# Optimization experiments

Hardware: AMD Instinct MI355X
Metric: run time of the kernel (lower is better)

## Reference

```python
import jax, jax.numpy as jnp
import numpy as np

K = 3
K2 = K * K
PAD = (K - 1) // 2
DECAY_RATE = 4.0
REL_THRESHOLD = 0.3
EPS = 1e-8


def _deform_sample(depth, offset):
    """Deformable bilinear gather equivalent to the fixed-identity-weight
    ModulatedDeformConv2d (mask=1, bias=0). Returns [B, K2, H, W]."""
    B, _, H, W = depth.shape
    d = depth[:, 0]  # [B, H, W]
    dt = depth.dtype
    # mmcv offset layout: channel 2*i = dy, 2*i+1 = dx for kernel point i
    off = offset.reshape(B, K2, 2, H, W)
    off_y, off_x = off[:, :, 0], off[:, :, 1]          # [B, K2, H, W]
    ky = (jnp.arange(K2) // K - PAD).astype(dt)        # [K2]
    kx = (jnp.arange(K2) % K - PAD).astype(dt)
    ys = jnp.arange(H, dtype=dt)
    xs = jnp.arange(W, dtype=dt)
    # sampling locations: p = base_pixel + kernel_offset + learned_offset
    py = off_y + ys[None, None, :, None] + ky[None, :, None, None]  # [B,K2,H,W]
    px = off_x + xs[None, None, None, :] + kx[None, :, None, None]
    y0 = jnp.floor(py)
    x0 = jnp.floor(px)
    wy = py - y0  # bilinear weights
    wx = px - x0
    y0i = y0.astype(jnp.int32)
    x0i = x0.astype(jnp.int32)

    def gather(iy, ix):
        # zero-padded gather (matches mmcv out-of-bounds handling)
        valid = (iy >= 0) & (iy < H) & (ix >= 0) & (ix < W)
        iyc = jnp.clip(iy, 0, H - 1)
        ixc = jnp.clip(ix, 0, W - 1)
        vals = jax.vmap(lambda img, a, b: img[a, b])(d, iyc, ixc)  # [B,K2,H,W]
        return jnp.where(valid, vals, jnp.zeros((), dt))

    v00 = gather(y0i, x0i)
    v01 = gather(y0i, x0i + 1)
    v10 = gather(y0i + 1, x0i)
    v11 = gather(y0i + 1, x0i + 1)
    return (v00 * (1 - wy) * (1 - wx) + v01 * (1 - wy) * wx
            + v10 * wy * (1 - wx) + v11 * wy * wx)


def setup_inputs() -> dict:
    key = jax.random.key(0)
    k1, k2 = jax.random.split(key)
    B, H, W = 8, 480, 640
    depth = jax.random.uniform(k1, (B, 1, H, W), dtype=jnp.float32)
    offset = jax.random.normal(k2, (B, 2 * K2, H, W), dtype=jnp.float32)
    return {"depth": depth, "offset": offset}


def reference(depth, offset):
    sampled = _deform_sample(depth, offset)           # [B, K2, H, W]
    center = sampled[:, K2 // 2: K2 // 2 + 1]         # [B, 1, H, W]
    depth_diff = jnp.abs(sampled - center)
    # normalize_mode == 'threshold' (default path)
    relative_diff = depth_diff / (center + EPS)
    within = relative_diff <= REL_THRESHOLD
    affinity = jnp.exp(-DECAY_RATE * (depth_diff - center * REL_THRESHOLD))
    return jnp.where(within, jnp.ones_like(affinity), affinity)
```

## Files before the change

### kernel.cpp

```cpp
#include <hip/hip_runtime.h>

constexpr int KK = 3;
constexpr int K2 = 9;
constexpr int PADC = 1;
constexpr float DECAY = 4.0f;
constexpr float RELT = 0.3f;
constexpr float EPSV = 1e-8f;
constexpr int H = 480;
constexpr int W = 640;
constexpr int HW = H * W;

typedef float f32x4 __attribute__((ext_vector_type(4)));

constexpr int TH = 16;
constexpr int TW = 64;
constexpr int PADT = 8;
constexpr int LR = TH + 2 * PADT;
constexpr int LC = TW + 2 * PADT;
constexpr int LSTRIDE = LC + 1;
constexpr int NSTAGE = LR * LC;

__device__ __forceinline__ float dsample(const float* __restrict__ img, int iy, int ix) {
    bool valid = (iy >= 0) & (iy < H) & (ix >= 0) & (ix < W);
    int iyc = min(max(iy, 0), H - 1);
    int ixc = min(max(ix, 0), W - 1);
    float v = img[iyc * W + ixc];
    return valid ? v : 0.0f;
}

__device__ __forceinline__ void tap4(const float* __restrict__ tile,
                                     const float* __restrict__ dimg,
                                     int by0, int bx0, int r, int col,
                                     f32x4 oy, f32x4 ox, int ky, int kx,
                                     float* s4) {
    int y0[4], x0[4];
    float wy[4], wx[4];
    bool fast = true;
#pragma unroll
    for (int j = 0; j < 4; ++j) {
        float pyt = oy[j] + (float)(r + PADT + ky);
        float pxt = ox[j] + (float)(col + j + PADT + kx);
        float y0f = floorf(pyt);
        float x0f = floorf(pxt);
        wy[j] = pyt - y0f;
        wx[j] = pxt - x0f;
        y0[j] = (int)y0f;
        x0[j] = (int)x0f;
        fast &= ((unsigned)y0[j] < (unsigned)(LR - 1)) & ((unsigned)x0[j] < (unsigned)(LC - 1));
    }
    if (fast) {
#pragma unroll
        for (int j = 0; j < 4; ++j) {
            int a = y0[j] * LSTRIDE + x0[j];
            float v00 = tile[a];
            float v01 = tile[a + 1];
            float v10 = tile[a + LSTRIDE];
            float v11 = tile[a + LSTRIDE + 1];
            float wy1 = 1.0f - wy[j];
            float wx1 = 1.0f - wx[j];
            s4[j] = v00 * wy1 * wx1 + v01 * wy1 * wx[j] + v10 * wy[j] * wx1 + v11 * wy[j] * wx[j];
        }
    } else {
#pragma unroll
        for (int j = 0; j < 4; ++j) {
            int gy = y0[j] + by0 - PADT;
            int gx = x0[j] + bx0 - PADT;
            float v00 = dsample(dimg, gy, gx);
            float v01 = dsample(dimg, gy, gx + 1);
            float v10 = dsample(dimg, gy + 1, gx);
            float v11 = dsample(dimg, gy + 1, gx + 1);
            float wy1 = 1.0f - wy[j];
            float wx1 = 1.0f - wx[j];
            s4[j] = v00 * wy1 * wx1 + v01 * wy1 * wx[j] + v10 * wy[j] * wx1 + v11 * wy[j] * wx[j];
        }
    }
}

__global__ __launch_bounds__(256) void affinity_kernel(
    const float* __restrict__ depth,
    const float* __restrict__ offset,
    float* __restrict__ out)
{
    const int bx0 = blockIdx.x * TW;
    const int by0 = blockIdx.y * TH;
    const int b   = blockIdx.z;
    const int t   = threadIdx.x;

    __shared__ float tile[LR * LSTRIDE];

    const float* __restrict__ dimg = depth + (size_t)b * HW;

    const int col = (t & 15) * 4;
    const int r   = t >> 4;
    const int y   = by0 + r;
    const int x   = bx0 + col;

    const size_t obase = ((size_t)b * 2 * K2) * HW + (size_t)y * W + x;
    const float* __restrict__ offp = offset + obase;

    constexpr int ORD[K2] = {4, 0, 1, 2, 3, 5, 6, 7, 8};

    f32x4 oyc = *reinterpret_cast<const f32x4*>(offp + (size_t)(2 * ORD[0]) * HW);
    f32x4 oxc = *reinterpret_cast<const f32x4*>(offp + (size_t)(2 * ORD[0] + 1) * HW);

#pragma unroll
    for (int i = 0; i < NSTAGE / 256; ++i) {
        int idx = t + i * 256;
        int rr = idx / LC;
        int cc = idx - rr * LC;
        int yi = by0 - PADT + rr;
        int xi = bx0 - PADT + cc;
        float v = 0.0f;
        if ((unsigned)yi < (unsigned)H && (unsigned)xi < (unsigned)W)
            v = dimg[yi * W + xi];
        tile[rr * LSTRIDE + cc] = v;
    }
    __syncthreads();

    float* __restrict__ outp = out + ((size_t)b * K2) * HW + (size_t)y * W + x;

    float c4[4], thr[4], cr[4];

#pragma unroll
    for (int i = 0; i < K2; ++i) {
        const int k = ORD[i];
        f32x4 oyn, oxn;
        if (i + 1 < K2) {
            oyn = *reinterpret_cast<const f32x4*>(offp + (size_t)(2 * ORD[i + 1]) * HW);
            oxn = *reinterpret_cast<const f32x4*>(offp + (size_t)(2 * ORD[i + 1] + 1) * HW);
        }

        float s4[4];
        tap4(tile, dimg, by0, bx0, r, col, oyc, oxc, k / KK - PADC, k % KK - PADC, s4);

        if (i == 0) {
#pragma unroll
            for (int j = 0; j < 4; ++j) {
                c4[j]  = s4[j];
                thr[j] = RELT * (s4[j] + EPSV);
                cr[j]  = RELT * s4[j];
            }
            f32x4 ones = {1.0f, 1.0f, 1.0f, 1.0f};
            __builtin_nontemporal_store(ones, reinterpret_cast<f32x4*>(outp + (size_t)4 * HW));
        } else {
            f32x4 vals;
#pragma unroll
            for (int j = 0; j < 4; ++j) {
                float diff = fabsf(s4[j] - c4[j]);
                float aff = __expf(-DECAY * (diff - cr[j]));
                vals[j] = (diff <= thr[j]) ? 1.0f : aff;
            }
            __builtin_nontemporal_store(vals, reinterpret_cast<f32x4*>(outp + (size_t)k * HW));
        }
        oyc = oyn;
        oxc = oxn;
    }
}

extern "C" void kernel_launch(void* const* d_in, const int* in_sizes, int n_in,
                              void* d_out, int out_size, void* d_ws, size_t ws_size,
                              hipStream_t stream) {
    const float* depth = (const float*)d_in[0];
    const float* offset = (const float*)d_in[1];
    float* out = (float*)d_out;

    int B = in_sizes[0] / HW;
    dim3 grid(W / TW, H / TH, B);
    affinity_kernel<<<grid, 256, 0, stream>>>(depth, offset, out);
}
```

Before: 50.14 us.

## Store depth tile as fp16 pairs in two parity planes for paired loads

The shared-memory depth tile now holds half2 pairs (x, x+1) in two planes chosen by column parity. Each bilinear tap therefore needs two 32-bit LDS reads instead of four. The cost is a staging pass that does twice the global reads, and an fp16 rounding of depth values that may break the accuracy tolerance, mostly at the relative-threshold comparison.

```diff
diff --git a/kernel.cpp b/kernel.cpp
--- a/kernel.cpp
+++ b/kernel.cpp
@@ -1,4 +1,5 @@
 #include <hip/hip_runtime.h>
+#include <hip/hip_fp16.h>
 
 constexpr int KK = 3;
 constexpr int K2 = 9;
@@ -17,8 +18,11 @@
 constexpr int PADT = 8;
 constexpr int LR = TH + 2 * PADT;
 constexpr int LC = TW + 2 * PADT;
-constexpr int LSTRIDE = LC + 1;
-constexpr int NSTAGE = LR * LC;
+
+constexpr int NP = 40;
+constexpr int SP = NP + 1;
+constexpr int PLANE = LR * SP;
+constexpr int NSLOT = 2 * LR * NP;
 
 __device__ __forceinline__ float dsample(const float* __restrict__ img, int iy, int ix) {
     bool valid = (iy >= 0) & (iy < H) & (ix >= 0) & (ix < W);
@@ -28,7 +32,7 @@
     return valid ? v : 0.0f;
 }
 
-__device__ __forceinline__ void tap4(const float* __restrict__ tile,
+__device__ __forceinline__ void tap4(const __half2* __restrict__ tile,
                                      const float* __restrict__ dimg,
                                      int by0, int bx0, int r, int col,
                                      f32x4 oy, f32x4 ox, int ky, int kx,
@@ -51,14 +55,13 @@
     if (fast) {
 #pragma unroll
         for (int j = 0; j < 4; ++j) {
-            int a = y0[j] * LSTRIDE + x0[j];
-            float v00 = tile[a];
-            float v01 = tile[a + 1];
-            float v10 = tile[a + LSTRIDE];
-            float v11 = tile[a + LSTRIDE + 1];
+            int p  = x0[j] & 1;
+            int a  = p * PLANE + y0[j] * SP + (x0[j] >> 1);
+            float2 f0 = __half22float2(tile[a]);
+            float2 f1 = __half22float2(tile[a + SP]);
             float wy1 = 1.0f - wy[j];
             float wx1 = 1.0f - wx[j];
-            s4[j] = v00 * wy1 * wx1 + v01 * wy1 * wx[j] + v10 * wy[j] * wx1 + v11 * wy[j] * wx[j];
+            s4[j] = f0.x * wy1 * wx1 + f0.y * wy1 * wx[j] + f1.x * wy[j] * wx1 + f1.y * wy[j] * wx[j];
         }
     } else {
 #pragma unroll
@@ -86,7 +89,7 @@
     const int b   = blockIdx.z;
     const int t   = threadIdx.x;
 
-    __shared__ float tile[LR * LSTRIDE];
+    __shared__ __half2 tile[2 * PLANE];
 
     const float* __restrict__ dimg = depth + (size_t)b * HW;
 
@@ -104,16 +107,20 @@
     f32x4 oxc = *reinterpret_cast<const f32x4*>(offp + (size_t)(2 * ORD[0] + 1) * HW);
 
 #pragma unroll
-    for (int i = 0; i < NSTAGE / 256; ++i) {
-        int idx = t + i * 256;
-        int rr = idx / LC;
-        int cc = idx - rr * LC;
-        int yi = by0 - PADT + rr;
-        int xi = bx0 - PADT + cc;
-        float v = 0.0f;
-        if ((unsigned)yi < (unsigned)H && (unsigned)xi < (unsigned)W)
-            v = dimg[yi * W + xi];
-        tile[rr * LSTRIDE + cc] = v;
+    for (int i = 0; i < NSLOT / 256; ++i) {
+        int s  = t + i * 256;
+        int pl = s / (LR * NP);
+        int rem = s - pl * (LR * NP);
+        int rr = rem / NP;
+        int xp = rem - rr * NP;
+        int gy = by0 - PADT + rr;
+        int gx = bx0 - PADT + 2 * xp + pl;
+        float va = 0.0f, vb = 0.0f;
+        bool yok = (unsigned)gy < (unsigned)H;
+        int rowb = gy * W;
+        if (yok & ((unsigned)gx < (unsigned)W))       va = dimg[rowb + gx];
+        if (yok & ((unsigned)(gx + 1) < (unsigned)W)) vb = dimg[rowb + gx + 1];
+        tile[pl * PLANE + rr * SP + xp] = __floats2half2_rn(va, vb);
     }
     __syncthreads();
 
```

Measured after the change: 54.35 us. 1.08x slower.

## Halve tile height and process two pixels per thread instead of four

Applied to the files above, without the earlier changes.

Shrinks the block tile from 16x64 to 8x64 and has each of 256 threads handle 2 adjacent pixels instead of 4, using 2-wide vector loads and nontemporal stores. The shared-memory staging loop gains a bounds guard because the smaller halo tile no longer divides evenly by 256. The aim is more blocks and more threads per pixel to hide gather and memory latency. The cost is a much larger relative halo to stage per block (24x80 for 512 pixels) and narrower memory transactions.

```diff
diff --git a/kernel.cpp b/kernel.cpp
--- a/kernel.cpp
+++ b/kernel.cpp
@@ -10,9 +10,9 @@
 constexpr int W = 640;
 constexpr int HW = H * W;
 
-typedef float f32x4 __attribute__((ext_vector_type(4)));
+typedef float f32x2 __attribute__((ext_vector_type(2)));
 
-constexpr int TH = 16;
+constexpr int TH = 8;
 constexpr int TW = 64;
 constexpr int PADT = 8;
 constexpr int LR = TH + 2 * PADT;
@@ -28,16 +28,16 @@
     return valid ? v : 0.0f;
 }
 
-__device__ __forceinline__ void tap4(const float* __restrict__ tile,
+__device__ __forceinline__ void tap2(const float* __restrict__ tile,
                                      const float* __restrict__ dimg,
                                      int by0, int bx0, int r, int col,
-                                     f32x4 oy, f32x4 ox, int ky, int kx,
-                                     float* s4) {
-    int y0[4], x0[4];
-    float wy[4], wx[4];
+                                     f32x2 oy, f32x2 ox, int ky, int kx,
+                                     float* s2) {
+    int y0[2], x0[2];
+    float wy[2], wx[2];
     bool fast = true;
 #pragma unroll
-    for (int j = 0; j < 4; ++j) {
+    for (int j = 0; j < 2; ++j) {
         float pyt = oy[j] + (float)(r + PADT + ky);
         float pxt = ox[j] + (float)(col + j + PADT + kx);
         float y0f = floorf(pyt);
@@ -50,7 +50,7 @@
     }
     if (fast) {
 #pragma unroll
-        for (int j = 0; j < 4; ++j) {
+        for (int j = 0; j < 2; ++j) {
             int a = y0[j] * LSTRIDE + x0[j];
             float v00 = tile[a];
             float v01 = tile[a + 1];
@@ -58,11 +58,11 @@
             float v11 = tile[a + LSTRIDE + 1];
             float wy1 = 1.0f - wy[j];
             float wx1 = 1.0f - wx[j];
-            s4[j] = v00 * wy1 * wx1 + v01 * wy1 * wx[j] + v10 * wy[j] * wx1 + v11 * wy[j] * wx[j];
+            s2[j] = v00 * wy1 * wx1 + v01 * wy1 * wx[j] + v10 * wy[j] * wx1 + v11 * wy[j] * wx[j];
         }
     } else {
 #pragma unroll
-        for (int j = 0; j < 4; ++j) {
+        for (int j = 0; j < 2; ++j) {
             int gy = y0[j] + by0 - PADT;
             int gx = x0[j] + bx0 - PADT;
             float v00 = dsample(dimg, gy, gx);
@@ -71,7 +71,7 @@
             float v11 = dsample(dimg, gy + 1, gx + 1);
             float wy1 = 1.0f - wy[j];
             float wx1 = 1.0f - wx[j];
-            s4[j] = v00 * wy1 * wx1 + v01 * wy1 * wx[j] + v10 * wy[j] * wx1 + v11 * wy[j] * wx[j];
+            s2[j] = v00 * wy1 * wx1 + v01 * wy1 * wx[j] + v10 * wy[j] * wx1 + v11 * wy[j] * wx[j];
         }
     }
 }
@@ -90,8 +90,8 @@
 
     const float* __restrict__ dimg = depth + (size_t)b * HW;
 
-    const int col = (t & 15) * 4;
-    const int r   = t >> 4;
+    const int col = (t & 31) * 2;
+    const int r   = t >> 5;
     const int y   = by0 + r;
     const int x   = bx0 + col;
 
@@ -100,57 +100,59 @@
 
     constexpr int ORD[K2] = {4, 0, 1, 2, 3, 5, 6, 7, 8};
 
-    f32x4 oyc = *reinterpret_cast<const f32x4*>(offp + (size_t)(2 * ORD[0]) * HW);
-    f32x4 oxc = *reinterpret_cast<const f32x4*>(offp + (size_t)(2 * ORD[0] + 1) * HW);
+    f32x2 oyc = *reinterpret_cast<const f32x2*>(offp + (size_t)(2 * ORD[0]) * HW);
+    f32x2 oxc = *reinterpret_cast<const f32x2*>(offp + (size_t)(2 * ORD[0] + 1) * HW);
 
 #pragma unroll
-    for (int i = 0; i < NSTAGE / 256; ++i) {
+    for (int i = 0; i < (NSTAGE + 255) / 256; ++i) {
         int idx = t + i * 256;
-        int rr = idx / LC;
-        int cc = idx - rr * LC;
-        int yi = by0 - PADT + rr;
-        int xi = bx0 - PADT + cc;
-        float v = 0.0f;
-        if ((unsigned)yi < (unsigned)H && (unsigned)xi < (unsigned)W)
-            v = dimg[yi * W + xi];
-        tile[rr * LSTRIDE + cc] = v;
+        if (idx < NSTAGE) {
+            int rr = idx / LC;
+            int cc = idx - rr * LC;
+            int yi = by0 - PADT + rr;
+            int xi = bx0 - PADT + cc;
+            float v = 0.0f;
+            if ((unsigned)yi < (unsigned)H && (unsigned)xi < (unsigned)W)
+                v = dimg[yi * W + xi];
+            tile[rr * LSTRIDE + cc] = v;
+        }
     }
     __syncthreads();
 
     float* __restrict__ outp = out + ((size_t)b * K2) * HW + (size_t)y * W + x;
 
-    float c4[4], thr[4], cr[4];
+    float c2[2], thr[2], cr[2];
 
 #pragma unroll
     for (int i = 0; i < K2; ++i) {
         const int k = ORD[i];
-        f32x4 oyn, oxn;
+        f32x2 oyn, oxn;
         if (i + 1 < K2) {
-            oyn = *reinterpret_cast<const f32x4*>(offp + (size_t)(2 * ORD[i + 1]) * HW);
-            oxn = *reinterpret_cast<const f32x4*>(offp + (size_t)(2 * ORD[i + 1] + 1) * HW);
+            oyn = *reinterpret_cast<const f32x2*>(offp + (size_t)(2 * ORD[i + 1]) * HW);
+            oxn = *reinterpret_cast<const f32x2*>(offp + (size_t)(2 * ORD[i + 1] + 1) * HW);
         }
 
-        float s4[4];
-        tap4(tile, dimg, by0, bx0, r, col, oyc, oxc, k / KK - PADC, k % KK - PADC, s4);
+        float s2[2];
+        tap2(tile, dimg, by0, bx0, r, col, oyc, oxc, k / KK - PADC, k % KK - PADC, s2);
 
         if (i == 0) {
 #pragma unroll
-            for (int j = 0; j < 4; ++j) {
-                c4[j]  = s4[j];
-                thr[j] = RELT * (s4[j] + EPSV);
-                cr[j]  = RELT * s4[j];
+            for (int j = 0; j < 2; ++j) {
+                c2[j]  = s2[j];
+                thr[j] = RELT * (s2[j] + EPSV);
+                cr[j]  = RELT * s2[j];
             }
-            f32x4 ones = {1.0f, 1.0f, 1.0f, 1.0f};
-            __builtin_nontemporal_store(ones, reinterpret_cast<f32x4*>(outp + (size_t)4 * HW));
+            f32x2 ones = {1.0f, 1.0f};
+            __builtin_nontemporal_store(ones, reinterpret_cast<f32x2*>(outp + (size_t)4 * HW));
         } else {
-            f32x4 vals;
+            f32x2 vals;
 #pragma unroll
-            for (int j = 0; j < 4; ++j) {
-                float diff = fabsf(s4[j] - c4[j]);
+            for (int j = 0; j < 2; ++j) {
+                float diff = fabsf(s2[j] - c2[j]);
                 float aff = __expf(-DECAY * (diff - cr[j]));
                 vals[j] = (diff <= thr[j]) ? 1.0f : aff;
             }
-            __builtin_nontemporal_store(vals, reinterpret_cast<f32x4*>(outp + (size_t)k * HW));
+            __builtin_nontemporal_store(vals, reinterpret_cast<f32x2*>(outp + (size_t)k * HW));
         }
         oyc = oyn;
         oxc = oxn;
```

Result: no change. 50.84 us (+1.4%).

## Store depth tile as paired float2 planes for single-load bilinear neighbours

Applied to the files above, without the earlier changes.

Rearranges the shared-memory depth tile into two planes of (x, x+1) float pairs, split by the parity of the start column. Each bilinear tap then reads two 8-byte LDS loads instead of four scalar loads. Tile staging now uses vectorised float4 global loads, with a fast interior path that skips bounds checks. Interpolation is rewritten as three FMAs in lerp form. The cost is twice the shared memory, which may lower occupancy, plus possible bank conflicts on the 8-byte loads.

```diff
diff --git a/kernel.cpp b/kernel.cpp
--- a/kernel.cpp
+++ b/kernel.cpp
@@ -10,6 +10,7 @@
 constexpr int W = 640;
 constexpr int HW = H * W;
 
+typedef float f32x2 __attribute__((ext_vector_type(2)));
 typedef float f32x4 __attribute__((ext_vector_type(4)));
 
 constexpr int TH = 16;
@@ -17,8 +18,10 @@
 constexpr int PADT = 8;
 constexpr int LR = TH + 2 * PADT;
 constexpr int LC = TW + 2 * PADT;
-constexpr int LSTRIDE = LC + 1;
-constexpr int NSTAGE = LR * LC;
+
+constexpr int NPAIR = 42;
+constexpr int PLANE = LR * NPAIR;
+constexpr int NCHUNK = LR * (LC / 4);
 
 __device__ __forceinline__ float dsample(const float* __restrict__ img, int iy, int ix) {
     bool valid = (iy >= 0) & (iy < H) & (ix >= 0) & (ix < W);
@@ -28,7 +31,7 @@
     return valid ? v : 0.0f;
 }
 
-__device__ __forceinline__ void tap4(const float* __restrict__ tile,
+__device__ __forceinline__ void tap4(const f32x2* __restrict__ tile,
                                      const float* __restrict__ dimg,
                                      int by0, int bx0, int r, int col,
                                      f32x4 oy, f32x4 ox, int ky, int kx,
@@ -51,14 +54,13 @@
     if (fast) {
 #pragma unroll
         for (int j = 0; j < 4; ++j) {
-            int a = y0[j] * LSTRIDE + x0[j];
-            float v00 = tile[a];
-            float v01 = tile[a + 1];
-            float v10 = tile[a + LSTRIDE];
-            float v11 = tile[a + LSTRIDE + 1];
-            float wy1 = 1.0f - wy[j];
-            float wx1 = 1.0f - wx[j];
-            s4[j] = v00 * wy1 * wx1 + v01 * wy1 * wx[j] + v10 * wy[j] * wx1 + v11 * wy[j] * wx[j];
+            int p = x0[j] & 1;
+            int a = p * PLANE + y0[j] * NPAIR + (x0[j] >> 1);
+            f32x2 top = tile[a];
+            f32x2 bot = tile[a + NPAIR];
+            float h0 = fmaf(wx[j], top.y - top.x, top.x);
+            float h1 = fmaf(wx[j], bot.y - bot.x, bot.x);
+            s4[j] = fmaf(wy[j], h1 - h0, h0);
         }
     } else {
 #pragma unroll
@@ -69,9 +71,9 @@
             float v01 = dsample(dimg, gy, gx + 1);
             float v10 = dsample(dimg, gy + 1, gx);
             float v11 = dsample(dimg, gy + 1, gx + 1);
-            float wy1 = 1.0f - wy[j];
-            float wx1 = 1.0f - wx[j];
-            s4[j] = v00 * wy1 * wx1 + v01 * wy1 * wx[j] + v10 * wy[j] * wx1 + v11 * wy[j] * wx[j];
+            float h0 = fmaf(wx[j], v01 - v00, v00);
+            float h1 = fmaf(wx[j], v11 - v10, v10);
+            s4[j] = fmaf(wy[j], h1 - h0, h0);
         }
     }
 }
@@ -86,7 +88,7 @@
     const int b   = blockIdx.z;
     const int t   = threadIdx.x;
 
-    __shared__ float tile[LR * LSTRIDE];
+    __shared__ f32x2 tile[2 * PLANE];
 
     const float* __restrict__ dimg = depth + (size_t)b * HW;
 
@@ -103,17 +105,41 @@
     f32x4 oyc = *reinterpret_cast<const f32x4*>(offp + (size_t)(2 * ORD[0]) * HW);
     f32x4 oxc = *reinterpret_cast<const f32x4*>(offp + (size_t)(2 * ORD[0] + 1) * HW);
 
+    const bool interior = (by0 >= PADT) && (by0 + TH + PADT <= H) &&
+                          (bx0 >= PADT) && (bx0 + (LC - PADT) + 4 <= W);
 #pragma unroll
-    for (int i = 0; i < NSTAGE / 256; ++i) {
+    for (int i = 0; i < 3; ++i) {
         int idx = t + i * 256;
-        int rr = idx / LC;
-        int cc = idx - rr * LC;
-        int yi = by0 - PADT + rr;
-        int xi = bx0 - PADT + cc;
-        float v = 0.0f;
-        if ((unsigned)yi < (unsigned)H && (unsigned)xi < (unsigned)W)
-            v = dimg[yi * W + xi];
-        tile[rr * LSTRIDE + cc] = v;
+        if (idx < NCHUNK) {
+            int rr = idx / (LC / 4);
+            int cx = idx - rr * (LC / 4);
+            int c0 = cx * 4;
+            f32x4 v;
+            float v4;
+            if (interior) {
+                const float* rowp = dimg + (size_t)(by0 - PADT + rr) * W + (bx0 - PADT);
+                v  = *reinterpret_cast<const f32x4*>(rowp + c0);
+                v4 = rowp[c0 + 4];
+            } else {
+                int gy = by0 - PADT + rr;
+                bool yok = (unsigned)gy < (unsigned)H;
+                const float* rowp = dimg + (size_t)min(max(gy, 0), H - 1) * W;
+                float e[5];
+#pragma unroll
+                for (int jj = 0; jj < 5; ++jj) {
+                    int gx = bx0 - PADT + c0 + jj;
+                    bool ok = yok & ((unsigned)gx < (unsigned)W);
+                    e[jj] = ok ? rowp[min(max(gx, 0), W - 1)] : 0.0f;
+                }
+                v = f32x4{e[0], e[1], e[2], e[3]};
+                v4 = e[4];
+            }
+            int pbase = rr * NPAIR + (c0 >> 1);
+            f32x4 p0 = {v.x, v.y, v.z, v.w};
+            f32x4 p1 = {v.y, v.z, v.w, v4};
+            *reinterpret_cast<f32x4*>(&tile[pbase]) = p0;
+            *reinterpret_cast<f32x4*>(&tile[PLANE + pbase]) = p1;
+        }
     }
     __syncthreads();
 
```

Measured after the change: 50.31 us. No clear change (+0.3%).
